# Kernel optimization log

Measured on AMD Instinct MI355X. Metric: run time of the kernel, lower is better.

## Reference

```python
import jax, jax.numpy as jnp
import numpy as np
from jax import lax

LB, UB = 0.0, 0.1
N_ITERS = 32  # fixed-point iterations for water-filling rebalance


def _conv(x, w, b):
    y = lax.conv_general_dilated(x, w, (1, 1), ((1, 1), (1, 1)),
                                 dimension_numbers=("NCHW", "OIHW", "NCHW"))
    return y + b[None, :, None, None]


def _maxpool2(x):
    return lax.reduce_window(x, -jnp.inf, lax.max, (1, 1, 2, 2), (1, 1, 2, 2), "VALID")


def _linear(x, w, b):
    return x @ w.T + b


def _gru(x_num, W_ih, W_hh, b_ih, b_hh):
    # x_num: [B, S, N]; torch GRU gate order r, z, n
    B = x_num.shape[0]
    H = W_hh.shape[1]
    xs = jnp.swapaxes(x_num, 0, 1)  # [S, B, N]

    def step(h, x_t):
        gi = x_t @ W_ih.T + b_ih            # [B, 3H]
        gh = h @ W_hh.T + b_hh              # [B, 3H]
        i_r, i_z, i_n = jnp.split(gi, 3, axis=-1)
        h_r, h_z, h_n = jnp.split(gh, 3, axis=-1)
        r = jax.nn.sigmoid(i_r + h_r)
        z = jax.nn.sigmoid(i_z + h_z)
        n = jnp.tanh(i_n + r * h_n)
        h_new = (1.0 - z) * n + z * h
        return h_new, None

    h0 = jnp.zeros((B, H), dtype=x_num.dtype)
    h_last, _ = lax.scan(step, h0, xs)
    return h_last


def _rebalance_one(w):
    # vectorized fixed-point version of the per-sample while-loop water-filling
    def body(carry, _):
        old, wc = carry
        leftover = jnp.sum(old - wc)
        mask = wc != UB
        s = jnp.sum(jnp.where(mask, wc, 0.0))
        gift = jnp.where(mask & (s > 0), leftover * wc / jnp.where(s > 0, s, 1.0), 0.0)
        new_old = wc + gift
        new_wc = jnp.clip(new_old, LB, UB)
        return (new_old, new_wc), None

    init = (w, jnp.clip(w, LB, UB))
    (_, wc), _ = lax.scan(body, init, None, length=N_ITERS)
    return wc


def setup_inputs() -> dict:
    key = jax.random.key(0)
    ks = jax.random.split(key, 16)
    B, S, N, H_IMG, W_IMG, HID = 16, 60, 50, 64, 60, 128
    fc_in = 64 * (H_IMG // 4) * (W_IMG // 4)  # 15360
    sc = 0.05
    return {
        "x_num": jax.random.normal(ks[0], (B, S, N), jnp.float32),
        "x_img": jax.random.uniform(ks[1], (B, N, H_IMG, W_IMG), jnp.float32),
        "conv1_w": jax.random.normal(ks[2], (32, 1, 3, 3), jnp.float32) * sc,
        "conv1_b": jnp.zeros((32,), jnp.float32),
        "conv2_w": jax.random.normal(ks[3], (64, 32, 3, 3), jnp.float32) * sc,
        "conv2_b": jnp.zeros((64,), jnp.float32),
        "fc1_w": jax.random.normal(ks[4], (64, fc_in), jnp.float32) * 0.01,
        "fc1_b": jnp.zeros((64,), jnp.float32),
        "fc_binary_w": jax.random.normal(ks[5], (1, 64), jnp.float32) * sc,
        "fc_binary_b": jnp.zeros((1,), jnp.float32),
        "fc2_w": jax.random.normal(ks[6], (128, 64), jnp.float32) * sc,
        "fc2_b": jnp.zeros((128,), jnp.float32),
        "W_ih": jax.random.normal(ks[7], (3 * HID, N), jnp.float32) * sc,
        "W_hh": jax.random.normal(ks[8], (3 * HID, HID), jnp.float32) * sc,
        "b_ih": jnp.zeros((3 * HID,), jnp.float32),
        "b_hh": jnp.zeros((3 * HID,), jnp.float32),
        "gru_fc_w": jax.random.normal(ks[9], (N, HID), jnp.float32) * sc,
        "gru_fc_b": jnp.zeros((N,), jnp.float32),
        "fusion_w": jax.random.normal(ks[10], (64, N + 128), jnp.float32) * sc,
        "fusion_b": jnp.zeros((64,), jnp.float32),
        "final_w": jax.random.normal(ks[11], (N, 64), jnp.float32) * sc,
        "final_b": jnp.zeros((N,), jnp.float32),
    }


def reference(x_num, x_img, conv1_w, conv1_b, conv2_w, conv2_b, fc1_w, fc1_b,
              fc_binary_w, fc_binary_b, fc2_w, fc2_b, W_ih, W_hh, b_ih, b_hh,
              gru_fc_w, gru_fc_b, fusion_w, fusion_b, final_w, final_b):
    B, S, N = x_num.shape
    # GRU branch: last hidden -> Linear -> [B, N]
    h_last = _gru(x_num, W_ih, W_hh, b_ih, b_hh)
    numerical_features = _linear(h_last, gru_fc_w, gru_fc_b)

    # CNN branch on per-stock chart images
    xi = x_img.reshape(B * N, 1, x_img.shape[2], x_img.shape[3])
    h = _maxpool2(jax.nn.relu(_conv(xi, conv1_w, conv1_b)))
    h = _maxpool2(jax.nn.relu(_conv(h, conv2_w, conv2_b)))
    h = h.reshape(B * N, -1)
    feats = jax.nn.relu(_linear(h, fc1_w, fc1_b))
    binary_pred = jax.nn.sigmoid(_linear(feats, fc_binary_w, fc_binary_b))
    cnn_features = _linear(feats, fc2_w, fc2_b).reshape(B, N, -1).mean(axis=1)

    fused = jax.nn.relu(_linear(jnp.concatenate([numerical_features, cnn_features], axis=1), fusion_w, fusion_b))
    w = jax.nn.softmax(_linear(fused, final_w, final_b), axis=1)
    portfolio_weights = jax.vmap(_rebalance_one)(w)
    return portfolio_weights, binary_pred.reshape(B, N)
```

## Files before the change

### kernel.cpp

```cpp
#include <hip/hip_runtime.h>
#include <hip/hip_bf16.h>
#include <hip/hip_fp16.h>

typedef unsigned short ushort_t;
typedef short short8_t __attribute__((ext_vector_type(8)));
typedef _Float16 half8_t __attribute__((ext_vector_type(8)));
typedef _Float16 h2 __attribute__((ext_vector_type(2)));
typedef float f32x4 __attribute__((ext_vector_type(4)));
typedef float f32x16 __attribute__((ext_vector_type(16)));

#define NBATCH 16
#define SEQ    60
#define NSTK   50
#define HID    128
#define G3     384
#define NIMG   800
#define IH     64
#define IW     60
#define P1H    32
#define P1W    30
#define P2C    64
#define FCIN   15360

#define OFF_WHHF   0u
#define OFF_WPREP  24576u
#define OFF_WFC1   33792u
#define OFF_GI     525312u
#define OFF_HLAST  893952u
#define OFF_POOL2  896000u
#define OFF_FC2O   7040000u
#define OFF_PART   7142400u
#define OFF_W1H    7961600u
#define WS_FLOATS  7961760u

#define E_WHH  49152
#define E_WPR  18432
#define E_FC1  983040
#define E_W1H  160
#define E_TOT  (E_WHH + E_WPR + E_FC1 + E_W1H)

struct __align__(16) ConvS {
    ushort_t pool1t[18][4][32][8];
    union {
        float    imgp[35][60];
        ushort_t pool2s[64][120];
    } u;
};
struct __align__(16) GruS {
    ushort_t hb[2][16 * 136];
};
#define SMEM_BYTES 52224

__device__ __forceinline__ float fast_sig(float x) {
    const float e = __expf(-x);
    return __builtin_amdgcn_rcpf(1.f + e);
}
__device__ __forceinline__ float fast_tanh(float x) {
    const float xc = fmaxf(fminf(x, 15.f), -15.f);
    const float e = __expf(2.f * xc);
    return (e - 1.f) * __builtin_amdgcn_rcpf(e + 1.f);
}
__device__ __forceinline__ h2 hmax2v(h2 a, h2 b) {
    h2 r;
    r[0] = a[0] > b[0] ? a[0] : b[0];
    r[1] = a[1] > b[1] ? a[1] : b[1];
    return r;
}

__global__ __launch_bounds__(384) void k_pre(const float* __restrict__ xnum,
                                             const float* __restrict__ wih,
                                             const float* __restrict__ bih,
                                             const float* __restrict__ whh,
                                             const float* __restrict__ c2w,
                                             const float* __restrict__ fc1w,
                                             const float* __restrict__ c1w,
                                             const float* __restrict__ c1b,
                                             float* __restrict__ GI,
                                             ushort_t* __restrict__ whhf,
                                             ushort_t* __restrict__ wprep,
                                             ushort_t* __restrict__ wfc1,
                                             unsigned int* __restrict__ w1h)
{
    const int bid = blockIdx.x;
    if (bid < 960) {
        const int s = bid >> 4, b = bid & 15;
        const int j = threadIdx.x;
        const float* xr = xnum + (size_t)(b * SEQ + s) * NSTK;
        const float* wr = wih + (size_t)j * NSTK;
        float a = bih[j];
        #pragma unroll 10
        for (int k = 0; k < NSTK; ++k) a = fmaf(xr[k], wr[k], a);
        GI[((size_t)s * 16 + b) * G3 + j] = a;
        return;
    }
    const int idx = (bid - 960) * 384 + threadIdx.x;
    if (idx < E_WHH) {
        const int e = idx;
        const int i = e & 7, l = (e >> 3) & 63, ksj = e >> 9;
        const int ks = ksj & 3, jt = ksj >> 2;
        const int j = jt * 16 + (l & 15);
        const int k = ks * 32 + ((l >> 4) << 3) + i;
        __hip_bfloat16 hv = __float2bfloat16(whh[j * HID + k]);
        whhf[e] = *(ushort_t*)&hv;
    } else if (idx < E_WHH + E_WPR) {
        const int e = idx - E_WHH;
        const int i = e & 7, l = (e >> 3) & 63, rest = e >> 9;
        const int ks = rest & 1, mt = rest >> 1;
        const int tap = mt % 9, mm = mt / 9;
        const int oc = mm * 32 + (l & 31);
        const int ic = ks * 16 + ((l >> 5) << 3) + i;
        const _Float16 hv = (_Float16)c2w[((size_t)oc * 32 + ic) * 9 + tap];
        wprep[e] = *(const ushort_t*)&hv;
    } else if (idx < E_WHH + E_WPR + E_FC1) {
        const int e = idx - (E_WHH + E_WPR);
        const int i = e & 7, l = (e >> 3) & 63, rest = e >> 9;
        const int n = rest & 3, T = rest >> 2;
        const int oc = n * 16 + (l & 15);
        const int k = T * 32 + ((l >> 4) << 3) + i;
        __hip_bfloat16 hv = __float2bfloat16(fc1w[(size_t)oc * FCIN + k]);
        wfc1[e] = *(ushort_t*)&hv;
    } else if (idx < E_TOT) {
        const int e = idx - (E_WHH + E_WPR + E_FC1);
        if (e < 144) {
            const int p = e / 9, tap = e - p * 9;
            const int ch0 = (p >> 2) * 8 + (p & 3) * 2;
            const _Float16 lo = (_Float16)c1w[ch0 * 9 + tap];
            const _Float16 hi = (_Float16)c1w[(ch0 + 1) * 9 + tap];
            w1h[p * 9 + tap] = ((unsigned)*(const ushort_t*)&hi << 16) | *(const ushort_t*)&lo;
        } else {
            const int p = e - 144;
            const int ch0 = (p >> 2) * 8 + (p & 3) * 2;
            const _Float16 lo = (_Float16)c1b[ch0];
            const _Float16 hi = (_Float16)c1b[ch0 + 1];
            w1h[144 + p] = ((unsigned)*(const ushort_t*)&hi << 16) | *(const ushort_t*)&lo;
        }
    }
}

__global__ __launch_bounds__(512, 2) void k_mega(const float* __restrict__ x_img,
                                                 const unsigned int* __restrict__ w1h,
                                                 const float* __restrict__ c2b,
                                                 const ushort_t* __restrict__ wprep,
                                                 const float* __restrict__ GI,
                                                 const ushort_t* __restrict__ whhf,
                                                 const float* __restrict__ bhh,
                                                 ushort_t* __restrict__ pool2,
                                                 float* __restrict__ hlast)
{
    extern __shared__ char smraw[];
    const int tid = threadIdx.x;
    const int bid = blockIdx.x;

    if (bid == 0) {
        GruS* g = (GruS*)smraw;
        const int w = tid >> 6, l = tid & 63;
        const int arow = l & 15, kq = l >> 4;
        const int hh = w * 16 + (l & 15);
        const int b0 = (l >> 4) * 4;
        short8_t wfr[3][4];
        #pragma unroll
        for (int g3 = 0; g3 < 3; ++g3)
            #pragma unroll
            for (int ks = 0; ks < 4; ++ks)
                wfr[g3][ks] = *(const short8_t*)&whhf[((((g3 * 8 + w) * 4 + ks) * 64 + l) * 8)];
        const float bhr = bhh[hh];
        const float bhz = bhh[128 + hh];
        const float bhn = bhh[256 + hh];
        float h[4] = {0.f, 0.f, 0.f, 0.f};
        for (int i = tid; i < 1088; i += 512) ((unsigned int*)g->hb[0])[i] = 0u;
        __syncthreads();

        int cur = 0;
        for (int s = 0; s < SEQ; ++s) {
            const float* gis = GI + ((size_t)s * 16 + b0) * G3 + hh;
            float cr[4], cz[4], cn[4];
            #pragma unroll
            for (int r = 0; r < 4; ++r) {
                cr[r] = gis[r * G3];
                cz[r] = gis[r * G3 + 128];
                cn[r] = gis[r * G3 + 256];
            }
            f32x4 ar = {0.f, 0.f, 0.f, 0.f};
            f32x4 az = {0.f, 0.f, 0.f, 0.f};
            f32x4 an = {0.f, 0.f, 0.f, 0.f};
            #pragma unroll
            for (int ks = 0; ks < 4; ++ks) {
                const short8_t af = *(const short8_t*)&g->hb[cur][arow * 136 + ks * 32 + kq * 8];
                ar = __builtin_amdgcn_mfma_f32_16x16x32_bf16(af, wfr[0][ks], ar, 0, 0, 0);
                az = __builtin_amdgcn_mfma_f32_16x16x32_bf16(af, wfr[1][ks], az, 0, 0, 0);
                an = __builtin_amdgcn_mfma_f32_16x16x32_bf16(af, wfr[2][ks], an, 0, 0, 0);
            }
            const int nxt = cur ^ 1;
            #pragma unroll
            for (int r = 0; r < 4; ++r) {
                const float rg = fast_sig(cr[r] + ar[r] + bhr);
                const float zg = fast_sig(cz[r] + az[r] + bhz);
                const float ng = fast_tanh(cn[r] + rg * (an[r] + bhn));
                h[r] = (1.f - zg) * ng + zg * h[r];
                __hip_bfloat16 t = __float2bfloat16(h[r]);
                g->hb[nxt][(b0 + r) * 136 + hh] = *(ushort_t*)&t;
            }
            __syncthreads();
            cur = nxt;
        }
        #pragma unroll
        for (int r = 0; r < 4; ++r) hlast[(b0 + r) * HID + hh] = h[r];
        return;
    }

    ConvS* c = (ConvS*)smraw;
    const int img  = (bid - 1) >> 1;
    const int half = (bid - 1) & 1;
    const float* xim = x_img + (size_t)img * (IH * IW);
    const int rowbase = 29 * half;

    {
        const short8_t z = {0, 0, 0, 0, 0, 0, 0, 0};
        const int zrow = half ? 17 : 0;
        if (tid < 128) {
            const int cg = tid >> 5, xs = tid & 31;
            *(short8_t*)&c->pool1t[zrow][cg][xs][0] = z;
        } else if (tid < 272) {
            const int q = tid - 128;
            const int ly = q / 8, cg = (q >> 1) & 3, xs = (q & 1) * 31;
            *(short8_t*)&c->pool1t[ly][cg][xs][0] = z;
        }
    }
    {
        const f32x4* src = (const f32x4*)(xim + rowbase * IW);
        f32x4* dst = (f32x4*)c->u.imgp;
        for (int i = tid; i < 525; i += 512) dst[i] = src[i];
    }
    __syncthreads();

    if (tid < 510) {
        const int gj = tid / 30, px = tid - gj * 30;
        const int g = half * 15 + gj;
        const int ly = gj + 1 - half;
        const h2 z2 = {(_Float16)0.f, (_Float16)0.f};
        h2 patch2[4][4];
        #pragma unroll
        for (int yy = 0; yy < 4; ++yy) {
            const int giy = 2 * g - 1 + yy;
            const int liy = giy - rowbase;
            #pragma unroll
            for (int xx = 0; xx < 4; ++xx) {
                const int ix = 2 * px - 1 + xx;
                const float v = (giy >= 0 && giy < IH && ix >= 0 && ix < IW)
                                    ? c->u.imgp[liy][ix] : 0.f;
                const _Float16 vh = (_Float16)v;
                h2 p2; p2[0] = vh; p2[1] = vh;
                patch2[yy][xx] = p2;
            }
        }
        #pragma unroll 1
        for (int cg = 0; cg < 4; ++cg) {
            unsigned int ov[4];
            #pragma unroll
            for (int pr = 0; pr < 4; ++pr) {
                const int p = cg * 4 + pr;
                h2 wv[9];
                #pragma unroll
                for (int t = 0; t < 9; ++t) {
                    const unsigned int wu = w1h[p * 9 + t];
                    wv[t] = *(const h2*)&wu;
                }
                h2 a00 = z2, a01 = z2, a10 = z2, a11 = z2;
                #pragma unroll
                for (int ky = 0; ky < 3; ++ky)
                    #pragma unroll
                    for (int kx = 0; kx < 3; ++kx) {
                        const h2 wt = wv[ky * 3 + kx];
                        a00 = wt * patch2[ky][kx]     + a00;
                        a01 = wt * patch2[ky][kx + 1] + a01;
                        a10 = wt * patch2[ky + 1][kx] + a10;
                        a11 = wt * patch2[ky + 1][kx + 1] + a11;
                    }
                const unsigned int bu = w1h[144 + p];
                const h2 bia2 = *(const h2*)&bu;
                h2 m = hmax2v(hmax2v(a00, a01), hmax2v(a10, a11));
                h2 r = hmax2v(m + bia2, z2);
                ov[pr] = *(unsigned int*)&r;
            }
            *(uint4*)&c->pool1t[ly][cg][px + 1][0] = *(uint4*)ov;
        }
    }
    __syncthreads();

    {
        const int w  = tid >> 6, l = tid & 63;
        const int m  = w & 1;
        const int hi = l >> 5;
        const int col = l & 31;

        half8_t af[9][2];
        #pragma unroll
        for (int tap = 0; tap < 9; ++tap)
            #pragma unroll
            for (int ks = 0; ks < 2; ++ks)
                af[tap][ks] = *(const half8_t*)&wprep[(((m * 9 + tap) * 2 + ks) * 64 + l) * 8];
        float bia[16];
        #pragma unroll
        for (int r = 0; r < 16; ++r)
            bia[r] = c2b[m * 32 + (r & 3) + 8 * (r >> 2) + 4 * hi];

        const bool wr = ((col & 1) == 0) && (col < 30);
        const int px = col >> 1;

        #pragma unroll 1
        for (int yy = 0; yy < 2; ++yy) {
            const int ypl = (w >> 1) + yy * 4;
            f32x16 a0, a1;
            #pragma unroll
            for (int r = 0; r < 16; ++r) { a0[r] = 0.f; a1[r] = 0.f; }
            #pragma unroll
            for (int ro = 0; ro < 4; ++ro) {
                const int ly = 2 * ypl + ro;
                half8_t bf[3][2];
                #pragma unroll
                for (int kx = 0; kx < 3; ++kx)
                    #pragma unroll
                    for (int ks = 0; ks < 2; ++ks)
                        bf[kx][ks] = *(const half8_t*)&c->pool1t[ly][ks * 2 + hi][kx + col][0];
                if (ro < 3) {
                    #pragma unroll
                    for (int kx = 0; kx < 3; ++kx)
                        #pragma unroll
                        for (int ks = 0; ks < 2; ++ks)
                            a0 = __builtin_amdgcn_mfma_f32_32x32x16_f16(af[ro * 3 + kx][ks], bf[kx][ks], a0, 0, 0, 0);
                }
                if (ro >= 1) {
                    #pragma unroll
                    for (int kx = 0; kx < 3; ++kx)
                        #pragma unroll
                        for (int ks = 0; ks < 2; ++ks)
                            a1 = __builtin_amdgcn_mfma_f32_32x32x16_f16(af[(ro - 1) * 3 + kx][ks], bf[kx][ks], a1, 0, 0, 0);
                }
            }
            #pragma unroll
            for (int r = 0; r < 16; ++r) {
                float v = fmaxf(a0[r], a1[r]);
                v = fmaxf(v, __shfl_xor(v, 1, 64));
                v = fmaxf(v + bia[r], 0.f);
                if (wr) {
                    const int oc = m * 32 + (r & 3) + 8 * (r >> 2) + 4 * hi;
                    __hip_bfloat16 hv = __float2bfloat16(v);
                    c->u.pool2s[oc][ypl * 15 + px] = *(ushort_t*)&hv;
                }
            }
        }
        __syncthreads();
        {
            int4* dst = (int4*)(pool2 + (size_t)img * FCIN);
            const int4* src = (const int4*)c->u.pool2s;
            #pragma unroll
            for (int jj = 0; jj < 2; ++jj) {
                const int i = tid + jj * 512;
                if (i < 960) {
                    const int oc = i / 15, cc = i - oc * 15;
                    dst[oc * 30 + half * 15 + cc] = src[i];
                }
            }
        }
    }
}

__global__ __launch_bounds__(256) void k_fc1(const ushort_t* __restrict__ pool2,
                                             const ushort_t* __restrict__ wfc1,
                                             float* __restrict__ part)
{
    const int mt = blockIdx.x >> 4;
    const int ks = blockIdx.x & 15;
    const int n = threadIdx.x >> 6, l = threadIdx.x & 63;
    const int arow = l & 15, kq = l >> 4;
    const int img16 = mt * 16;
    const ushort_t* Ab = pool2 + (size_t)(img16 + arow) * FCIN + ks * 960 + kq * 8;
    const ushort_t* Bb = wfc1 + ((size_t)(ks * 30 * 4 + n) * 64 + l) * 8;
    f32x4 acc0 = {0.f, 0.f, 0.f, 0.f}, acc1 = {0.f, 0.f, 0.f, 0.f};
    #pragma unroll 10
    for (int t = 0; t < 30; t += 2) {
        const short8_t aA = *(const short8_t*)(Ab + (size_t)t * 32);
        const short8_t bA = *(const short8_t*)(Bb + (size_t)t * 2048);
        const short8_t aB = *(const short8_t*)(Ab + (size_t)(t + 1) * 32);
        const short8_t bB = *(const short8_t*)(Bb + (size_t)(t + 1) * 2048);
        acc0 = __builtin_amdgcn_mfma_f32_16x16x32_bf16(aA, bA, acc0, 0, 0, 0);
        acc1 = __builtin_amdgcn_mfma_f32_16x16x32_bf16(aB, bB, acc1, 0, 0, 0);
    }
    float* dst = &part[((size_t)ks * NIMG + img16 + kq * 4) * 64 + n * 16 + arow];
    #pragma unroll
    for (int r = 0; r < 4; ++r)
        dst[(size_t)r * 64] = acc0[r] + acc1[r];
}

__device__ __forceinline__ float wave_sum(float v) {
    #pragma unroll
    for (int o = 32; o > 0; o >>= 1) v += __shfl_xor(v, o, 64);
    return v;
}
__device__ __forceinline__ float wave_max(float v) {
    #pragma unroll
    for (int o = 32; o > 0; o >>= 1) v = fmaxf(v, __shfl_xor(v, o, 64));
    return v;
}

__global__ __launch_bounds__(512) void k_post(const float* __restrict__ part,
                                              const float* __restrict__ fc1b,
                                              const float* __restrict__ fbw,
                                              const float* __restrict__ fbb,
                                              const float* __restrict__ fc2w,
                                              const float* __restrict__ fc2b,
                                              float* __restrict__ out,
                                              float* __restrict__ fc2o)
{
    const int t = threadIdx.x;
    const int im8 = t >> 6;
    const int tl = t & 63;
    const int img = blockIdx.x * 8 + im8;
    float s = fc1b[tl];
    #pragma unroll
    for (int ks = 0; ks < 16; ++ks) s += part[((size_t)ks * NIMG + img) * 64 + tl];
    const float f = fmaxf(s, 0.f);
    __shared__ float flc[8][64];
    flc[im8][tl] = f;
    const float bs = wave_sum(f * fbw[tl]);
    if (tl == 0) out[800 + img] = 1.f / (1.f + expf(-(bs + fbb[0])));
    __syncthreads();
    #pragma unroll
    for (int q = 0; q < 2; ++q) {
        const int j = tl + q * 64;
        float a2 = fc2b[j];
        #pragma unroll 8
        for (int k = 0; k < 64; ++k) a2 = fmaf(flc[im8][k], fc2w[j * 64 + k], a2);
        fc2o[(size_t)img * 128 + j] = a2;
    }
}

__global__ __launch_bounds__(64) void k_final(const float* __restrict__ hlast,
                                              const float* __restrict__ fc2o,
                                              const float* __restrict__ gw,
                                              const float* __restrict__ gb,
                                              const float* __restrict__ fw,
                                              const float* __restrict__ fb,
                                              const float* __restrict__ finw,
                                              const float* __restrict__ finb,
                                              float* __restrict__ out)
{
    const int b = blockIdx.x, t = threadIdx.x;
    __shared__ float cf[128], nf[64], fu[64];
    #pragma unroll
    for (int jj = 0; jj < 2; ++jj) {
        const int j = t + jj * 64;
        float s = 0.f;
        for (int n = 0; n < NSTK; ++n) s += fc2o[(size_t)(b * NSTK + n) * 128 + j];
        cf[j] = s * (1.0f / 50.0f);
    }
    float s = 0.f;
    if (t < NSTK) {
        s = gb[t];
        for (int k = 0; k < HID; ++k) s = fmaf(hlast[b * HID + k], gw[t * HID + k], s);
    }
    nf[t] = (t < NSTK) ? s : 0.f;
    __syncthreads();
    float f = fb[t];
    for (int k = 0; k < NSTK; ++k) f = fmaf(nf[k], fw[t * 178 + k], f);
    for (int k = 0; k < 128; ++k) f = fmaf(cf[k], fw[t * 178 + 50 + k], f);
    fu[t] = fmaxf(f, 0.f);
    __syncthreads();
    float L = -3.4e38f;
    if (t < NSTK) {
        L = finb[t];
        for (int k = 0; k < 64; ++k) L = fmaf(fu[k], finw[t * 64 + k], L);
    }
    const float m = wave_max(L);
    const float e = (t < NSTK) ? expf(L - m) : 0.f;
    const float se = wave_sum(e);
    const float wv = e / se;
    float old = wv;
    float wc = fminf(fmaxf(wv, 0.f), 0.1f);
    for (int it = 0; it < 32; ++it) {
        const float leftover = wave_sum(old - wc);
        const bool mask = (wc != 0.1f);
        const float ssum = wave_sum(mask ? wc : 0.f);
        const float gift = (mask && ssum > 0.f) ? leftover * wc / ssum : 0.f;
        old = wc + gift;
        wc = fminf(fmaxf(old, 0.f), 0.1f);
    }
    if (t < NSTK) out[b * NSTK + t] = wc;
}

extern "C" void kernel_launch(void* const* d_in, const int* in_sizes, int n_in,
                              void* d_out, int out_size, void* d_ws, size_t ws_size,
                              hipStream_t stream)
{
    const float* x_num = (const float*)d_in[0];
    const float* x_img = (const float*)d_in[1];
    const float* c1w  = (const float*)d_in[2];
    const float* c1b  = (const float*)d_in[3];
    const float* c2w  = (const float*)d_in[4];
    const float* c2b  = (const float*)d_in[5];
    const float* fc1w = (const float*)d_in[6];
    const float* fc1b = (const float*)d_in[7];
    const float* fbw  = (const float*)d_in[8];
    const float* fbb  = (const float*)d_in[9];
    const float* fc2w = (const float*)d_in[10];
    const float* fc2b = (const float*)d_in[11];
    const float* wih  = (const float*)d_in[12];
    const float* whh  = (const float*)d_in[13];
    const float* bih  = (const float*)d_in[14];
    const float* bhh  = (const float*)d_in[15];
    const float* gw   = (const float*)d_in[16];
    const float* gb   = (const float*)d_in[17];
    const float* fw   = (const float*)d_in[18];
    const float* fb   = (const float*)d_in[19];
    const float* finw = (const float*)d_in[20];
    const float* finb = (const float*)d_in[21];
    float* out = (float*)d_out;
    float* ws  = (float*)d_ws;
    if (ws_size < (size_t)WS_FLOATS * 4) return;

    ushort_t* whhf  = (ushort_t*)(ws + OFF_WHHF);
    ushort_t* wprep = (ushort_t*)(ws + OFF_WPREP);
    ushort_t* wfc1  = (ushort_t*)(ws + OFF_WFC1);
    float* GI       = ws + OFF_GI;
    float* hlast    = ws + OFF_HLAST;
    ushort_t* pool2 = (ushort_t*)(ws + OFF_POOL2);
    float* fc2o     = ws + OFF_FC2O;
    float* part     = ws + OFF_PART;
    unsigned int* w1h = (unsigned int*)(ws + OFF_W1H);

    (void)hipFuncSetAttribute(reinterpret_cast<const void*>(k_mega),
                              hipFuncAttributeMaxDynamicSharedMemorySize, SMEM_BYTES);

    k_pre   <<<960 + 2737, 384, 0, stream>>>(x_num, wih, bih, whh, c2w, fc1w, c1w, c1b,
                                             GI, whhf, wprep, wfc1, w1h);
    k_mega  <<<2 * NIMG + 1, 512, SMEM_BYTES, stream>>>(x_img, w1h, c2b, wprep,
                                                        GI, whhf, bhh, pool2, hlast);
    k_fc1   <<<50 * 16, 256, 0, stream>>>(pool2, wfc1, part);
    k_post  <<<100, 512, 0, stream>>>(part, fc1b, fbw, fbb, fc2w, fc2b, out, fc2o);
    k_final <<<NBATCH, 64, 0, stream>>>(hlast, fc2o, gw, gb, fw, fb, finw, finb, out);
}
```

Before: 140.9 us.

## Transpose fc2 weights, split k_post per image, widen k_final, unroll conv loops

k_pre gains a step that writes a transposed copy of fc2 weights to workspace. k_post then runs one 64-thread block per image and reads those weights with coalesced loads instead of strided ones. k_final uses 256 threads, splitting the 50-stock mean into two halves and staging hlast in shared memory. Two conv loops in k_mega lose their unroll-1 pragmas and become fully unrolled, which may raise register pressure under launch_bounds(512,2).

```diff
diff --git a/kernel.cpp b/kernel.cpp
--- a/kernel.cpp
+++ b/kernel.cpp
@@ -31,13 +31,15 @@
 #define OFF_FC2O   7040000u
 #define OFF_PART   7142400u
 #define OFF_W1H    7961600u
-#define WS_FLOATS  7961760u
+#define OFF_FC2WT  7961760u
+#define WS_FLOATS  7969952u
 
 #define E_WHH  49152
 #define E_WPR  18432
 #define E_FC1  983040
 #define E_W1H  160
-#define E_TOT  (E_WHH + E_WPR + E_FC1 + E_W1H)
+#define E_FT   8192
+#define E_TOT  (E_WHH + E_WPR + E_FC1 + E_W1H + E_FT)
 
 struct __align__(16) ConvS {
     ushort_t pool1t[18][4][32][8];
@@ -75,11 +77,13 @@
                                              const float* __restrict__ fc1w,
                                              const float* __restrict__ c1w,
                                              const float* __restrict__ c1b,
+                                             const float* __restrict__ fc2w,
                                              float* __restrict__ GI,
                                              ushort_t* __restrict__ whhf,
                                              ushort_t* __restrict__ wprep,
                                              ushort_t* __restrict__ wfc1,
-                                             unsigned int* __restrict__ w1h)
+                                             unsigned int* __restrict__ w1h,
+                                             float* __restrict__ fc2wT)
 {
     const int bid = blockIdx.x;
     if (bid < 960) {
@@ -119,7 +123,7 @@
         const int k = T * 32 + ((l >> 4) << 3) + i;
         __hip_bfloat16 hv = __float2bfloat16(fc1w[(size_t)oc * FCIN + k]);
         wfc1[e] = *(ushort_t*)&hv;
-    } else if (idx < E_TOT) {
+    } else if (idx < E_WHH + E_WPR + E_FC1 + E_W1H) {
         const int e = idx - (E_WHH + E_WPR + E_FC1);
         if (e < 144) {
             const int p = e / 9, tap = e - p * 9;
@@ -134,6 +138,10 @@
             const _Float16 hi = (_Float16)c1b[ch0 + 1];
             w1h[144 + p] = ((unsigned)*(const ushort_t*)&hi << 16) | *(const ushort_t*)&lo;
         }
+    } else if (idx < E_TOT) {
+        const int e = idx - (E_WHH + E_WPR + E_FC1 + E_W1H);
+        const int j = e & 127, k = e >> 7;
+        fc2wT[e] = fc2w[j * 64 + k];
     }
 }
 
@@ -253,7 +261,7 @@
                 patch2[yy][xx] = p2;
             }
         }
-        #pragma unroll 1
+        #pragma unroll
         for (int cg = 0; cg < 4; ++cg) {
             unsigned int ov[4];
             #pragma unroll
@@ -307,7 +315,7 @@
         const bool wr = ((col & 1) == 0) && (col < 30);
         const int px = col >> 1;
 
-        #pragma unroll 1
+        #pragma unroll
         for (int yy = 0; yy < 2; ++yy) {
             const int ypl = (w >> 1) + yy * 4;
             f32x16 a0, a1;
@@ -403,89 +411,103 @@
     return v;
 }
 
-__global__ __launch_bounds__(512) void k_post(const float* __restrict__ part,
-                                              const float* __restrict__ fc1b,
-                                              const float* __restrict__ fbw,
-                                              const float* __restrict__ fbb,
-                                              const float* __restrict__ fc2w,
-                                              const float* __restrict__ fc2b,
-                                              float* __restrict__ out,
-                                              float* __restrict__ fc2o)
+__global__ __launch_bounds__(64) void k_post(const float* __restrict__ part,
+                                             const float* __restrict__ fc1b,
+                                             const float* __restrict__ fbw,
+                                             const float* __restrict__ fbb,
+                                             const float* __restrict__ fc2wT,
+                                             const float* __restrict__ fc2b,
+                                             float* __restrict__ out,
+                                             float* __restrict__ fc2o)
 {
-    const int t = threadIdx.x;
-    const int im8 = t >> 6;
-    const int tl = t & 63;
-    const int img = blockIdx.x * 8 + im8;
-    float s = fc1b[tl];
+    const int img = blockIdx.x, t = threadIdx.x;
+    float s = fc1b[t];
     #pragma unroll
-    for (int ks = 0; ks < 16; ++ks) s += part[((size_t)ks * NIMG + img) * 64 + tl];
+    for (int ks = 0; ks < 16; ++ks) s += part[((size_t)ks * NIMG + img) * 64 + t];
     const float f = fmaxf(s, 0.f);
-    __shared__ float flc[8][64];
-    flc[im8][tl] = f;
-    const float bs = wave_sum(f * fbw[tl]);
-    if (tl == 0) out[800 + img] = 1.f / (1.f + expf(-(bs + fbb[0])));
+    __shared__ float fl[64];
+    fl[t] = f;
+    const float bs = wave_sum(f * fbw[t]);
+    if (t == 0) out[800 + img] = 1.f / (1.f + expf(-(bs + fbb[0])));
     __syncthreads();
-    #pragma unroll
-    for (int q = 0; q < 2; ++q) {
-        const int j = tl + q * 64;
-        float a2 = fc2b[j];
-        #pragma unroll 8
-        for (int k = 0; k < 64; ++k) a2 = fmaf(flc[im8][k], fc2w[j * 64 + k], a2);
-        fc2o[(size_t)img * 128 + j] = a2;
-    }
-}
-
-__global__ __launch_bounds__(64) void k_final(const float* __restrict__ hlast,
-                                              const float* __restrict__ fc2o,
-                                              const float* __restrict__ gw,
-                                              const float* __restrict__ gb,
-                                              const float* __restrict__ fw,
-                                              const float* __restrict__ fb,
-                                              const float* __restrict__ finw,
-                                              const float* __restrict__ finb,
-                                              float* __restrict__ out)
+    float a0 = fc2b[t], a1 = fc2b[t + 64];
+    #pragma unroll 8
+    for (int k = 0; k < 64; ++k) {
+        const float fk = fl[k];
+        a0 = fmaf(fk, fc2wT[k * 128 + t], a0);
+        a1 = fmaf(fk, fc2wT[k * 128 + 64 + t], a1);
+    }
+    fc2o[(size_t)img * 128 + t] = a0;
+    fc2o[(size_t)img * 128 + 64 + t] = a1;
+}
+
+__global__ __launch_bounds__(256) void k_final(const float* __restrict__ hlast,
+                                               const float* __restrict__ fc2o,
+                                               const float* __restrict__ gw,
+                                               const float* __restrict__ gb,
+                                               const float* __restrict__ fw,
+                                               const float* __restrict__ fb,
+                                               const float* __restrict__ finw,
+                                               const float* __restrict__ finb,
+                                               float* __restrict__ out)
 {
     const int b = blockIdx.x, t = threadIdx.x;
-    __shared__ float cf[128], nf[64], fu[64];
-    #pragma unroll
-    for (int jj = 0; jj < 2; ++jj) {
-        const int j = t + jj * 64;
+    __shared__ float cfp[2][128], nf[64], fu[64], hl[128];
+    if (t < 128) hl[t] = hlast[b * HID + t];
+    {
+        const int j = t & 127, hf = t >> 7;
+        const float* base = fc2o + ((size_t)(b * NSTK + hf * 25) * 128) + j;
         float s = 0.f;
-        for (int n = 0; n < NSTK; ++n) s += fc2o[(size_t)(b * NSTK + n) * 128 + j];
-        cf[j] = s * (1.0f / 50.0f);
-    }
-    float s = 0.f;
-    if (t < NSTK) {
-        s = gb[t];
-        for (int k = 0; k < HID; ++k) s = fmaf(hlast[b * HID + k], gw[t * HID + k], s);
-    }
-    nf[t] = (t < NSTK) ? s : 0.f;
+        #pragma unroll 5
+        for (int n = 0; n < 25; ++n) s += base[(size_t)n * 128];
+        cfp[hf][j] = s;
+    }
     __syncthreads();
-    float f = fb[t];
-    for (int k = 0; k < NSTK; ++k) f = fmaf(nf[k], fw[t * 178 + k], f);
-    for (int k = 0; k < 128; ++k) f = fmaf(cf[k], fw[t * 178 + 50 + k], f);
-    fu[t] = fmaxf(f, 0.f);
+    if (t < 64) {
+        float s = 0.f;
+        if (t < NSTK) {
+            s = gb[t];
+            #pragma unroll 8
+            for (int k = 0; k < HID; ++k) s = fmaf(hl[k], gw[t * HID + k], s);
+        }
+        nf[t] = (t < NSTK) ? s : 0.f;
+    }
     __syncthreads();
-    float L = -3.4e38f;
-    if (t < NSTK) {
-        L = finb[t];
-        for (int k = 0; k < 64; ++k) L = fmaf(fu[k], finw[t * 64 + k], L);
-    }
-    const float m = wave_max(L);
-    const float e = (t < NSTK) ? expf(L - m) : 0.f;
-    const float se = wave_sum(e);
-    const float wv = e / se;
-    float old = wv;
-    float wc = fminf(fmaxf(wv, 0.f), 0.1f);
-    for (int it = 0; it < 32; ++it) {
-        const float leftover = wave_sum(old - wc);
-        const bool mask = (wc != 0.1f);
-        const float ssum = wave_sum(mask ? wc : 0.f);
-        const float gift = (mask && ssum > 0.f) ? leftover * wc / ssum : 0.f;
-        old = wc + gift;
-        wc = fminf(fmaxf(old, 0.f), 0.1f);
-    }
-    if (t < NSTK) out[b * NSTK + t] = wc;
+    if (t < 64) {
+        float f = fb[t];
+        #pragma unroll 10
+        for (int k = 0; k < NSTK; ++k) f = fmaf(nf[k], fw[t * 178 + k], f);
+        #pragma unroll 8
+        for (int k = 0; k < 128; ++k) {
+            const float cfk = (cfp[0][k] + cfp[1][k]) * (1.0f / 50.0f);
+            f = fmaf(cfk, fw[t * 178 + 50 + k], f);
+        }
+        fu[t] = fmaxf(f, 0.f);
+    }
+    __syncthreads();
+    if (t < 64) {
+        float L = -3.4e38f;
+        if (t < NSTK) {
+            L = finb[t];
+            #pragma unroll 8
+            for (int k = 0; k < 64; ++k) L = fmaf(fu[k], finw[t * 64 + k], L);
+        }
+        const float m = wave_max(L);
+        const float e = (t < NSTK) ? expf(L - m) : 0.f;
+        const float se = wave_sum(e);
+        const float wv = e / se;
+        float old = wv;
+        float wc = fminf(fmaxf(wv, 0.f), 0.1f);
+        for (int it = 0; it < 32; ++it) {
+            const float leftover = wave_sum(old - wc);
+            const bool mask = (wc != 0.1f);
+            const float ssum = wave_sum(mask ? wc : 0.f);
+            const float gift = (mask && ssum > 0.f) ? leftover * wc / ssum : 0.f;
+            old = wc + gift;
+            wc = fminf(fmaxf(old, 0.f), 0.1f);
+        }
+        if (t < NSTK) out[b * NSTK + t] = wc;
+    }
 }
 
 extern "C" void kernel_launch(void* const* d_in, const int* in_sizes, int n_in,
@@ -527,15 +549,16 @@
     float* fc2o     = ws + OFF_FC2O;
     float* part     = ws + OFF_PART;
     unsigned int* w1h = (unsigned int*)(ws + OFF_W1H);
+    float* fc2wT    = ws + OFF_FC2WT;
 
     (void)hipFuncSetAttribute(reinterpret_cast<const void*>(k_mega),
                               hipFuncAttributeMaxDynamicSharedMemorySize, SMEM_BYTES);
 
-    k_pre   <<<960 + 2737, 384, 0, stream>>>(x_num, wih, bih, whh, c2w, fc1w, c1w, c1b,
-                                             GI, whhf, wprep, wfc1, w1h);
+    k_pre   <<<960 + 2758, 384, 0, stream>>>(x_num, wih, bih, whh, c2w, fc1w, c1w, c1b, fc2w,
+                                             GI, whhf, wprep, wfc1, w1h, fc2wT);
     k_mega  <<<2 * NIMG + 1, 512, SMEM_BYTES, stream>>>(x_img, w1h, c2b, wprep,
                                                         GI, whhf, bhh, pool2, hlast);
     k_fc1   <<<50 * 16, 256, 0, stream>>>(pool2, wfc1, part);
-    k_post  <<<100, 512, 0, stream>>>(part, fc1b, fbw, fbb, fc2w, fc2b, out, fc2o);
-    k_final <<<NBATCH, 64, 0, stream>>>(hlast, fc2o, gw, gb, fw, fb, finw, finb, out);
-}
+    k_post  <<<NIMG, 64, 0, stream>>>(part, fc1b, fbw, fbb, fc2wT, fc2b, out, fc2o);
+    k_final <<<NBATCH, 256, 0, stream>>>(hlast, fc2o, gw, gb, fw, fb, finw, finb, out);
+}
```

After: 137.6 us. 1.02x faster.
